# Kernel tuning notes

Measured on AMD Instinct MI355X. Metric: run time of the kernel, lower is better.

The kernel has to match this reference:

```python
import jax, jax.numpy as jnp
import numpy as np

D_MODEL = 1024
N_HEADS = 16


def setup_inputs() -> dict:
    key0 = jax.random.key(0)
    ks = jax.random.split(key0, 13)
    B, Lq, Lk, D = 2, 1024, 2048, D_MODEL
    scale = 0.02
    inp = {
        "query": jax.random.normal(ks[0], (B, Lq, D), jnp.float32),
        "key": jax.random.normal(ks[1], (B, Lk, D), jnp.float32),
        "value": jax.random.normal(ks[2], (B, Lk, D), jnp.float32),
        "mask": jax.random.randint(ks[3], (B, 1, Lq, Lk), 0, 2, jnp.int32),
        "attn_bias": jax.random.normal(ks[4], (B, N_HEADS, Lq, Lk), jnp.float32) * 0.1,
        "Wq": jax.random.normal(ks[5], (D, D), jnp.float32) * scale,
        "bq": jnp.zeros((D,), jnp.float32),
        "Wk": jax.random.normal(ks[6], (D, D), jnp.float32) * scale,
        "bk": jnp.zeros((D,), jnp.float32),
        "Wv": jax.random.normal(ks[7], (D, D), jnp.float32) * scale,
        "bv": jnp.zeros((D,), jnp.float32),
        "Wo": jax.random.normal(ks[8], (D, D), jnp.float32) * scale,
        "bo": jnp.zeros((D,), jnp.float32),
    }
    return inp


def reference(query, key, value, mask, attn_bias, Wq, bq, Wk, bk, Wv, bv, Wo, bo):
    B, Lq, D = query.shape
    Lk = key.shape[1]
    H = N_HEADS
    dh = D // H
    # projections (torch Linear: x @ W.T + b), then split heads -> [B,H,L,dh]
    Q = (query @ Wq.T + bq).reshape(B, Lq, H, dh).transpose(0, 2, 1, 3)
    K = (key @ Wk.T + bk).reshape(B, Lk, H, dh).transpose(0, 2, 1, 3)
    V = (value @ Wv.T + bv).reshape(B, Lk, H, dh).transpose(0, 2, 1, 3)
    scores = jnp.einsum("bhqd,bhkd->bhqk", Q, K) / jnp.sqrt(jnp.float32(dh))
    scores = scores + attn_bias
    scores = jnp.where(mask == 0, jnp.float32(-1e9), scores)
    attn = jax.nn.softmax(scores, axis=-1)  # dropout disabled (eval / p=0)
    out = jnp.einsum("bhqk,bhkd->bhqd", attn, V)
    out = out.transpose(0, 2, 1, 3).reshape(B, Lq, D)
    out = out @ Wo.T + bo
    return out, attn
```

## Files before the change

### kernel.cpp

```cpp
#include <hip/hip_runtime.h>
#include <hip/hip_bf16.h>

typedef __hip_bfloat16 bf16;
typedef __bf16  bf16x8 __attribute__((ext_vector_type(8)));
typedef float   f32x4  __attribute__((ext_vector_type(4)));

static constexpr int DMODEL = 1024;
static constexpr int NHEADS = 16;
static constexpr int DHEAD  = 64;
static constexpr int BATCH  = 2;
static constexpr int SLQ    = 1024;
static constexpr int SLK    = 2048;
static constexpr size_t OUTQ = (size_t)BATCH * SLQ * DMODEL;

__device__ __forceinline__ void stage8(unsigned short* dst, const bf16* src) {
    *(int4*)dst = *(const int4*)src;
}
__device__ __forceinline__ void stage8(unsigned short* dst, const float* src) {
    const float4 a = *(const float4*)(src);
    const float4 b = *(const float4*)(src + 4);
    bf16 h[8];
    h[0] = __float2bfloat16(a.x); h[1] = __float2bfloat16(a.y);
    h[2] = __float2bfloat16(a.z); h[3] = __float2bfloat16(a.w);
    h[4] = __float2bfloat16(b.x); h[5] = __float2bfloat16(b.y);
    h[6] = __float2bfloat16(b.z); h[7] = __float2bfloat16(b.w);
    *(int4*)dst = *(const int4*)h;
}

__device__ __forceinline__ void store_one(bf16* p, float v) { *p = __float2bfloat16(v); }
__device__ __forceinline__ void store_one(float* p, float v) { *p = v; }

template <typename TA, typename TB>
__device__ __forceinline__ void gemm_core(const TA* __restrict__ At, int lda,
                                          const TB* __restrict__ Bt, int ldb,
                                          int K, f32x4 acc[2][2])
{
    __shared__ __align__(16) unsigned short As[64][40];
    __shared__ __align__(16) unsigned short Bs[64][40];
    const int tid  = threadIdx.x;
    const int lane = tid & 63;
    const int wave = tid >> 6;
    const int wr   = (wave >> 1) * 32;
    const int wc   = (wave & 1) * 32;
    const int lrow = lane & 15;
    const int koff = (lane >> 4) * 8;
    const int srow   = tid >> 2;
    const int schunk = (tid & 3) * 8;

    for (int kt = 0; kt < K; kt += 32) {
        stage8(&As[srow][schunk], At + (size_t)srow * lda + kt + schunk);
        stage8(&Bs[srow][schunk], Bt + (size_t)srow * ldb + kt + schunk);
        __syncthreads();
        bf16x8 a0 = *(const bf16x8*)(&As[wr      + lrow][koff]);
        bf16x8 a1 = *(const bf16x8*)(&As[wr + 16 + lrow][koff]);
        bf16x8 b0 = *(const bf16x8*)(&Bs[wc      + lrow][koff]);
        bf16x8 b1 = *(const bf16x8*)(&Bs[wc + 16 + lrow][koff]);
        acc[0][0] = __builtin_amdgcn_mfma_f32_16x16x32_bf16(a0, b0, acc[0][0], 0, 0, 0);
        acc[0][1] = __builtin_amdgcn_mfma_f32_16x16x32_bf16(a0, b1, acc[0][1], 0, 0, 0);
        acc[1][0] = __builtin_amdgcn_mfma_f32_16x16x32_bf16(a1, b0, acc[1][0], 0, 0, 0);
        acc[1][1] = __builtin_amdgcn_mfma_f32_16x16x32_bf16(a1, b1, acc[1][1], 0, 0, 0);
        __syncthreads();
    }
}

template <typename TA, typename TC>
__global__ __launch_bounds__(256)
void k_proj(const TA* __restrict__ A, const float* __restrict__ W,
            const float* __restrict__ bias, TC* __restrict__ C, int K, int N)
{
    const int m0 = blockIdx.x * 64;
    const int n0 = blockIdx.y * 64;
    f32x4 z = {0.f, 0.f, 0.f, 0.f};
    f32x4 acc[2][2] = {{z, z}, {z, z}};
    gemm_core(A + (size_t)m0 * K, K, W + (size_t)n0 * K, K, K, acc);
    const int lane = threadIdx.x & 63;
    const int wave = threadIdx.x >> 6;
    const int wr = (wave >> 1) * 32, wc = (wave & 1) * 32;
#pragma unroll
    for (int i = 0; i < 2; ++i)
#pragma unroll
        for (int j = 0; j < 2; ++j) {
            const int col = n0 + wc + j * 16 + (lane & 15);
            const float bv = bias[col];
#pragma unroll
            for (int r = 0; r < 4; ++r) {
                const int row = m0 + wr + i * 16 + (lane >> 4) * 4 + r;
                store_one(&C[(size_t)row * N + col], acc[i][j][r] + bv);
            }
        }
}

__global__ __launch_bounds__(256)
void k_projV(const float* __restrict__ A, const float* __restrict__ W,
             const float* __restrict__ bias, bf16* __restrict__ Vt)
{
    const int m0 = blockIdx.x * 64;
    const int n0 = blockIdx.y * 64;
    f32x4 z = {0.f, 0.f, 0.f, 0.f};
    f32x4 acc[2][2] = {{z, z}, {z, z}};
    gemm_core(A + (size_t)m0 * DMODEL, DMODEL, W + (size_t)n0 * DMODEL, DMODEL, DMODEL, acc);
    const int lane = threadIdx.x & 63;
    const int wave = threadIdx.x >> 6;
    const int wr = (wave >> 1) * 32, wc = (wave & 1) * 32;
#pragma unroll
    for (int i = 0; i < 2; ++i)
#pragma unroll
        for (int j = 0; j < 2; ++j) {
            const int col = n0 + wc + j * 16 + (lane & 15);
            const float bv = bias[col];
            const int h = col >> 6, d = col & 63;
            const int mb = m0 + wr + i * 16 + (lane >> 4) * 4;
            const int b = mb >> 11;
            const int kk = mb & 2047;
            bf16* dst = Vt + ((size_t)(b * NHEADS + h) * DHEAD + d) * SLK + kk;
#pragma unroll
            for (int r = 0; r < 4; ++r)
                dst[r] = __float2bfloat16(acc[i][j][r] + bv);
        }
}

__global__ __launch_bounds__(256)
void k_attn(const bf16* __restrict__ Qp, const bf16* __restrict__ Kp,
            const float* __restrict__ bias, const int* __restrict__ mask,
            const bf16* __restrict__ Vt, float* __restrict__ attn,
            bf16* __restrict__ ctx)
{
    constexpr int SST = 2052;
    constexpr int PST = 520;

    __shared__ __align__(16) float S[16 * SST];
    __shared__ __align__(16) bf16  Pc[16 * PST];
    __shared__ float wmax[4][16], wsum[4][16];
    __shared__ float m_s[16], inv_s[16];

    const int qt = blockIdx.x, bh = blockIdx.y;
    const int b = bh >> 4, h = bh & 15;
    const int q0 = qt * 16;
    const int tid  = threadIdx.x;
    const int lane = tid & 63, w = tid >> 6;
    const int lr = lane & 15, lk = lane >> 4;

    const bf16* qb = Qp + ((size_t)(b * SLQ + q0 + lr)) * DMODEL + h * DHEAD + lk * 8;
    const bf16x8 a0 = *(const bf16x8*)qb;
    const bf16x8 a1 = *(const bf16x8*)(qb + 32);

    const bf16* kb = Kp + (size_t)b * SLK * DMODEL + h * DHEAD + lk * 8;
#pragma unroll 4
    for (int ct = 0; ct < 32; ++ct) {
        const int c0 = w * 512 + ct * 16;
        const bf16* kp = kb + (size_t)(c0 + lr) * DMODEL;
        bf16x8 b0 = *(const bf16x8*)kp;
        bf16x8 b1 = *(const bf16x8*)(kp + 32);
        f32x4 acc = {0.f, 0.f, 0.f, 0.f};
        acc = __builtin_amdgcn_mfma_f32_16x16x32_bf16(a0, b0, acc, 0, 0, 0);
        acc = __builtin_amdgcn_mfma_f32_16x16x32_bf16(a1, b1, acc, 0, 0, 0);
#pragma unroll
        for (int r = 0; r < 4; ++r)
            S[(lk * 4 + r) * SST + c0 + lr] = acc[r] * 0.125f;
    }

    for (int r = 0; r < 16; ++r) {
        float* sp = &S[r * SST + w * 512];
        const size_t brow = ((size_t)bh * SLQ + q0 + r) * SLK + w * 512 + lane * 4;
        const size_t mrow = ((size_t)b  * SLQ + q0 + r) * SLK + w * 512 + lane * 4;
        f32x4 v0 = *(const f32x4*)(sp + lane * 4);
        f32x4 v1 = *(const f32x4*)(sp + 256 + lane * 4);
        const float4 bb0 = *(const float4*)(bias + brow);
        const float4 bb1 = *(const float4*)(bias + brow + 256);
        const int4 mm0 = *(const int4*)(mask + mrow);
        const int4 mm1 = *(const int4*)(mask + mrow + 256);
        float s0 = (mm0.x == 0) ? -1e9f : v0[0] + bb0.x;
        float s1 = (mm0.y == 0) ? -1e9f : v0[1] + bb0.y;
        float s2 = (mm0.z == 0) ? -1e9f : v0[2] + bb0.z;
        float s3 = (mm0.w == 0) ? -1e9f : v0[3] + bb0.w;
        float s4 = (mm1.x == 0) ? -1e9f : v1[0] + bb1.x;
        float s5 = (mm1.y == 0) ? -1e9f : v1[1] + bb1.y;
        float s6 = (mm1.z == 0) ? -1e9f : v1[2] + bb1.z;
        float s7 = (mm1.w == 0) ? -1e9f : v1[3] + bb1.w;
        f32x4 w0 = {s0, s1, s2, s3};
        f32x4 w1 = {s4, s5, s6, s7};
        *(f32x4*)(sp + lane * 4)       = w0;
        *(f32x4*)(sp + 256 + lane * 4) = w1;

        float mx = fmaxf(fmaxf(fmaxf(s0, s1), fmaxf(s2, s3)),
                         fmaxf(fmaxf(s4, s5), fmaxf(s6, s7)));
        float l = __expf(s0 - mx) + __expf(s1 - mx) + __expf(s2 - mx) + __expf(s3 - mx)
                + __expf(s4 - mx) + __expf(s5 - mx) + __expf(s6 - mx) + __expf(s7 - mx);
        float mw = mx;
#pragma unroll
        for (int d = 1; d < 64; d <<= 1) mw = fmaxf(mw, __shfl_xor(mw, d));
        float lw = l * __expf(mx - mw);
#pragma unroll
        for (int d = 1; d < 64; d <<= 1) lw += __shfl_xor(lw, d);
        if (lane == 0) { wmax[w][r] = mw; wsum[w][r] = lw; }
    }
    __syncthreads();
    if (tid < 16) {
        const float m = fmaxf(fmaxf(wmax[0][tid], wmax[1][tid]),
                              fmaxf(wmax[2][tid], wmax[3][tid]));
        const float l = wsum[0][tid] * __expf(wmax[0][tid] - m)
                      + wsum[1][tid] * __expf(wmax[1][tid] - m)
                      + wsum[2][tid] * __expf(wmax[2][tid] - m)
                      + wsum[3][tid] * __expf(wmax[3][tid] - m);
        m_s[tid]   = m;
        inv_s[tid] = 1.0f / l;
    }
    __syncthreads();

    f32x4 pv = {0.f, 0.f, 0.f, 0.f};
    const bf16* vb = Vt + (size_t)bh * DHEAD * SLK + (size_t)(w * 16 + lr) * SLK + lk * 8;
    const int trow = tid >> 7;
    const int tcol = (tid & 127) * 4;
    for (int c = 0; c < 4; ++c) {
        const int ck0 = c * 512;
#pragma unroll
        for (int rp = 0; rp < 8; ++rp) {
            const int row = rp * 2 + trow;
            const f32x4 sv = *(const f32x4*)&S[row * SST + ck0 + tcol];
            const float m = m_s[row], inv = inv_s[row];
            const float p0 = __expf(sv[0] - m) * inv;
            const float p1 = __expf(sv[1] - m) * inv;
            const float p2 = __expf(sv[2] - m) * inv;
            const float p3 = __expf(sv[3] - m) * inv;
            const f32x4 pf = {p0, p1, p2, p3};
            __builtin_nontemporal_store(pf,
                (f32x4*)(attn + ((size_t)bh * SLQ + q0 + row) * SLK + ck0 + tcol));
            bf16 t4[4] = {__float2bfloat16(p0), __float2bfloat16(p1),
                          __float2bfloat16(p2), __float2bfloat16(p3)};
            *(int2*)&Pc[row * PST + tcol] = *(const int2*)t4;
        }
        __syncthreads();
        const bf16* vc = vb + ck0;
#pragma unroll
        for (int ks = 0; ks < 16; ++ks) {
            bf16x8 pa = *(const bf16x8*)&Pc[lr * PST + ks * 32 + lk * 8];
            bf16x8 vv = *(const bf16x8*)(vc + ks * 32);
            pv = __builtin_amdgcn_mfma_f32_16x16x32_bf16(pa, vv, pv, 0, 0, 0);
        }
        __syncthreads();
    }

    const int d = w * 16 + lr;
#pragma unroll
    for (int r = 0; r < 4; ++r) {
        const int q = lk * 4 + r;
        ctx[((size_t)(b * SLQ + q0 + q)) * DMODEL + h * DHEAD + d] =
            __float2bfloat16(pv[r]);
    }
}

extern "C" void kernel_launch(void* const* d_in, const int* in_sizes, int n_in,
                              void* d_out, int out_size, void* d_ws, size_t ws_size,
                              hipStream_t stream)
{
    const float* query = (const float*)d_in[0];
    const float* key   = (const float*)d_in[1];
    const float* value = (const float*)d_in[2];
    const int*   mask  = (const int*)d_in[3];
    const float* bias  = (const float*)d_in[4];
    const float* Wq = (const float*)d_in[5];
    const float* bq = (const float*)d_in[6];
    const float* Wk = (const float*)d_in[7];
    const float* bk = (const float*)d_in[8];
    const float* Wv = (const float*)d_in[9];
    const float* bv = (const float*)d_in[10];
    const float* Wo = (const float*)d_in[11];
    const float* bo = (const float*)d_in[12];

    float* out  = (float*)d_out;
    float* attn = out + OUTQ;

    bf16* Qp  = (bf16*)d_ws;
    bf16* ctx = (bf16*)d_ws;
    bf16* Kp  = (bf16*)d_out;
    bf16* Vt  = (bf16*)d_ws + (size_t)4 * 1024 * 1024;

    dim3 blk(256);

    k_proj<float, bf16><<<dim3(BATCH * SLQ / 64, DMODEL / 64), blk, 0, stream>>>(query, Wq, bq, Qp, DMODEL, DMODEL);
    k_proj<float, bf16><<<dim3(BATCH * SLK / 64, DMODEL / 64), blk, 0, stream>>>(key,   Wk, bk, Kp, DMODEL, DMODEL);
    k_projV<<<dim3(BATCH * SLK / 64, DMODEL / 64), blk, 0, stream>>>(value, Wv, bv, Vt);
    k_attn<<<dim3(SLQ / 16, BATCH * NHEADS), blk, 0, stream>>>(Qp, Kp, bias, mask, Vt, attn, ctx);
    k_proj<bf16, float><<<dim3(BATCH * SLQ / 64, DMODEL / 64), blk, 0, stream>>>(ctx, Wo, bo, out, DMODEL, DMODEL);
}
```

Before: 823.6 us.

## Run attention kernel with 1024 threads, one wave per query row

The attention block grows from 4 to 16 waves. Each wave computes a 128-column slice of QK^T, then owns one full query row for the bias, mask and softmax, which removes the cross-wave max/sum merge. The PV product is split across 4 K-groups per output d-slice, and the partial sums are reduced through shared memory. This raises parallelism per block to hide memory latency on the large bias, mask and attn traffic. In exchange it adds an extra reduction pass and barrier, and the __launch_bounds__(1024, 4) setting constrains registers.

```diff
diff --git a/kernel.cpp b/kernel.cpp
--- a/kernel.cpp
+++ b/kernel.cpp
@@ -119,7 +119,7 @@
         }
 }
 
-__global__ __launch_bounds__(256)
+__global__ __launch_bounds__(1024, 4)
 void k_attn(const bf16* __restrict__ Qp, const bf16* __restrict__ Kp,
             const float* __restrict__ bias, const int* __restrict__ mask,
             const bf16* __restrict__ Vt, float* __restrict__ attn,
@@ -130,7 +130,6 @@
 
     __shared__ __align__(16) float S[16 * SST];
     __shared__ __align__(16) bf16  Pc[16 * PST];
-    __shared__ float wmax[4][16], wsum[4][16];
     __shared__ float m_s[16], inv_s[16];
 
     const int qt = blockIdx.x, bh = blockIdx.y;
@@ -145,9 +144,9 @@
     const bf16x8 a1 = *(const bf16x8*)(qb + 32);
 
     const bf16* kb = Kp + (size_t)b * SLK * DMODEL + h * DHEAD + lk * 8;
-#pragma unroll 4
-    for (int ct = 0; ct < 32; ++ct) {
-        const int c0 = w * 512 + ct * 16;
+#pragma unroll 2
+    for (int ct = 0; ct < 8; ++ct) {
+        const int c0 = w * 128 + ct * 16;
         const bf16* kp = kb + (size_t)(c0 + lr) * DMODEL;
         bf16x8 b0 = *(const bf16x8*)kp;
         bf16x8 b1 = *(const bf16x8*)(kp + 32);
@@ -158,94 +157,93 @@
         for (int r = 0; r < 4; ++r)
             S[(lk * 4 + r) * SST + c0 + lr] = acc[r] * 0.125f;
     }
-
-    for (int r = 0; r < 16; ++r) {
-        float* sp = &S[r * SST + w * 512];
-        const size_t brow = ((size_t)bh * SLQ + q0 + r) * SLK + w * 512 + lane * 4;
-        const size_t mrow = ((size_t)b  * SLQ + q0 + r) * SLK + w * 512 + lane * 4;
-        f32x4 v0 = *(const f32x4*)(sp + lane * 4);
-        f32x4 v1 = *(const f32x4*)(sp + 256 + lane * 4);
-        const float4 bb0 = *(const float4*)(bias + brow);
-        const float4 bb1 = *(const float4*)(bias + brow + 256);
-        const int4 mm0 = *(const int4*)(mask + mrow);
-        const int4 mm1 = *(const int4*)(mask + mrow + 256);
-        float s0 = (mm0.x == 0) ? -1e9f : v0[0] + bb0.x;
-        float s1 = (mm0.y == 0) ? -1e9f : v0[1] + bb0.y;
-        float s2 = (mm0.z == 0) ? -1e9f : v0[2] + bb0.z;
-        float s3 = (mm0.w == 0) ? -1e9f : v0[3] + bb0.w;
-        float s4 = (mm1.x == 0) ? -1e9f : v1[0] + bb1.x;
-        float s5 = (mm1.y == 0) ? -1e9f : v1[1] + bb1.y;
-        float s6 = (mm1.z == 0) ? -1e9f : v1[2] + bb1.z;
-        float s7 = (mm1.w == 0) ? -1e9f : v1[3] + bb1.w;
-        f32x4 w0 = {s0, s1, s2, s3};
-        f32x4 w1 = {s4, s5, s6, s7};
-        *(f32x4*)(sp + lane * 4)       = w0;
-        *(f32x4*)(sp + 256 + lane * 4) = w1;
-
-        float mx = fmaxf(fmaxf(fmaxf(s0, s1), fmaxf(s2, s3)),
-                         fmaxf(fmaxf(s4, s5), fmaxf(s6, s7)));
-        float l = __expf(s0 - mx) + __expf(s1 - mx) + __expf(s2 - mx) + __expf(s3 - mx)
-                + __expf(s4 - mx) + __expf(s5 - mx) + __expf(s6 - mx) + __expf(s7 - mx);
-        float mw = mx;
-#pragma unroll
-        for (int d = 1; d < 64; d <<= 1) mw = fmaxf(mw, __shfl_xor(mw, d));
-        float lw = l * __expf(mx - mw);
-#pragma unroll
-        for (int d = 1; d < 64; d <<= 1) lw += __shfl_xor(lw, d);
-        if (lane == 0) { wmax[w][r] = mw; wsum[w][r] = lw; }
-    }
     __syncthreads();
-    if (tid < 16) {
-        const float m = fmaxf(fmaxf(wmax[0][tid], wmax[1][tid]),
-                              fmaxf(wmax[2][tid], wmax[3][tid]));
-        const float l = wsum[0][tid] * __expf(wmax[0][tid] - m)
-                      + wsum[1][tid] * __expf(wmax[1][tid] - m)
-                      + wsum[2][tid] * __expf(wmax[2][tid] - m)
-                      + wsum[3][tid] * __expf(wmax[3][tid] - m);
-        m_s[tid]   = m;
-        inv_s[tid] = 1.0f / l;
+
+    {
+        float* sp = &S[w * SST];
+        const size_t brow = ((size_t)bh * SLQ + q0 + w) * SLK;
+        const size_t mrow = ((size_t)b  * SLQ + q0 + w) * SLK;
+        float mx = -3.0e38f;
+#pragma unroll 2
+        for (int j = 0; j < 8; ++j) {
+            const int col = j * 256 + lane * 4;
+            f32x4 v = *(const f32x4*)(sp + col);
+            const float4 bb = *(const float4*)(bias + brow + col);
+            const int4  mm = *(const int4*)(mask + mrow + col);
+            float s0 = (mm.x == 0) ? -1e9f : v[0] + bb.x;
+            float s1 = (mm.y == 0) ? -1e9f : v[1] + bb.y;
+            float s2 = (mm.z == 0) ? -1e9f : v[2] + bb.z;
+            float s3 = (mm.w == 0) ? -1e9f : v[3] + bb.w;
+            f32x4 wv = {s0, s1, s2, s3};
+            *(f32x4*)(sp + col) = wv;
+            mx = fmaxf(mx, fmaxf(fmaxf(s0, s1), fmaxf(s2, s3)));
+        }
+#pragma unroll
+        for (int d = 1; d < 64; d <<= 1) mx = fmaxf(mx, __shfl_xor(mx, d));
+        float l = 0.f;
+#pragma unroll 2
+        for (int j = 0; j < 8; ++j) {
+            const int col = j * 256 + lane * 4;
+            const f32x4 v = *(const f32x4*)(sp + col);
+            l += __expf(v[0] - mx) + __expf(v[1] - mx)
+               + __expf(v[2] - mx) + __expf(v[3] - mx);
+        }
+#pragma unroll
+        for (int d = 1; d < 64; d <<= 1) l += __shfl_xor(l, d);
+        if (lane == 0) { m_s[w] = mx; inv_s[w] = 1.0f / l; }
     }
     __syncthreads();
 
     f32x4 pv = {0.f, 0.f, 0.f, 0.f};
-    const bf16* vb = Vt + (size_t)bh * DHEAD * SLK + (size_t)(w * 16 + lr) * SLK + lk * 8;
-    const int trow = tid >> 7;
-    const int tcol = (tid & 127) * 4;
+    const int g = w >> 2, dg = w & 3;
+    const bf16* vb = Vt + (size_t)bh * DHEAD * SLK + (size_t)(dg * 16 + lr) * SLK + lk * 8;
     for (int c = 0; c < 4; ++c) {
         const int ck0 = c * 512;
-#pragma unroll
-        for (int rp = 0; rp < 8; ++rp) {
-            const int row = rp * 2 + trow;
-            const f32x4 sv = *(const f32x4*)&S[row * SST + ck0 + tcol];
-            const float m = m_s[row], inv = inv_s[row];
-            const float p0 = __expf(sv[0] - m) * inv;
-            const float p1 = __expf(sv[1] - m) * inv;
-            const float p2 = __expf(sv[2] - m) * inv;
-            const float p3 = __expf(sv[3] - m) * inv;
-            const f32x4 pf = {p0, p1, p2, p3};
-            __builtin_nontemporal_store(pf,
-                (f32x4*)(attn + ((size_t)bh * SLQ + q0 + row) * SLK + ck0 + tcol));
-            bf16 t4[4] = {__float2bfloat16(p0), __float2bfloat16(p1),
-                          __float2bfloat16(p2), __float2bfloat16(p3)};
-            *(int2*)&Pc[row * PST + tcol] = *(const int2*)t4;
+        {
+            const int scol = lane * 8;
+            const float m = m_s[w], inv = inv_s[w];
+            const f32x4 s0 = *(const f32x4*)&S[w * SST + ck0 + scol];
+            const f32x4 s1 = *(const f32x4*)&S[w * SST + ck0 + scol + 4];
+            const f32x4 p0 = {__expf(s0[0] - m) * inv, __expf(s0[1] - m) * inv,
+                              __expf(s0[2] - m) * inv, __expf(s0[3] - m) * inv};
+            const f32x4 p1 = {__expf(s1[0] - m) * inv, __expf(s1[1] - m) * inv,
+                              __expf(s1[2] - m) * inv, __expf(s1[3] - m) * inv};
+            float* ap = attn + ((size_t)bh * SLQ + q0 + w) * SLK + ck0 + scol;
+            __builtin_nontemporal_store(p0, (f32x4*)ap);
+            __builtin_nontemporal_store(p1, (f32x4*)(ap + 4));
+            bf16 t8[8] = {__float2bfloat16(p0[0]), __float2bfloat16(p0[1]),
+                          __float2bfloat16(p0[2]), __float2bfloat16(p0[3]),
+                          __float2bfloat16(p1[0]), __float2bfloat16(p1[1]),
+                          __float2bfloat16(p1[2]), __float2bfloat16(p1[3])};
+            *(int4*)&Pc[w * PST + scol] = *(const int4*)t8;
         }
         __syncthreads();
         const bf16* vc = vb + ck0;
 #pragma unroll
-        for (int ks = 0; ks < 16; ++ks) {
-            bf16x8 pa = *(const bf16x8*)&Pc[lr * PST + ks * 32 + lk * 8];
-            bf16x8 vv = *(const bf16x8*)(vc + ks * 32);
+        for (int i = 0; i < 4; ++i) {
+            const int koff = (g * 4 + i) * 32;
+            bf16x8 pa = *(const bf16x8*)&Pc[lr * PST + koff + lk * 8];
+            bf16x8 vv = *(const bf16x8*)(vc + koff);
             pv = __builtin_amdgcn_mfma_f32_16x16x32_bf16(pa, vv, pv, 0, 0, 0);
         }
         __syncthreads();
     }
 
-    const int d = w * 16 + lr;
-#pragma unroll
-    for (int r = 0; r < 4; ++r) {
-        const int q = lk * 4 + r;
-        ctx[((size_t)(b * SLQ + q0 + q)) * DMODEL + h * DHEAD + d] =
-            __float2bfloat16(pv[r]);
+    float* rbuf = S;
+    *(f32x4*)&rbuf[(w * 64 + lane) * 4] = pv;
+    __syncthreads();
+    if (g == 0) {
+        f32x4 t = {0.f, 0.f, 0.f, 0.f};
+#pragma unroll
+        for (int gg = 0; gg < 4; ++gg)
+            t += *(const f32x4*)&rbuf[((gg * 4 + dg) * 64 + lane) * 4];
+        const int d = dg * 16 + lr;
+#pragma unroll
+        for (int r = 0; r < 4; ++r) {
+            const int q = lk * 4 + r;
+            ctx[((size_t)(b * SLQ + q0 + q)) * DMODEL + h * DHEAD + d] =
+                __float2bfloat16(t[r]);
+        }
     }
 }
 
@@ -280,6 +278,6 @@
     k_proj<float, bf16><<<dim3(BATCH * SLQ / 64, DMODEL / 64), blk, 0, stream>>>(query, Wq, bq, Qp, DMODEL, DMODEL);
     k_proj<float, bf16><<<dim3(BATCH * SLK / 64, DMODEL / 64), blk, 0, stream>>>(key,   Wk, bk, Kp, DMODEL, DMODEL);
     k_projV<<<dim3(BATCH * SLK / 64, DMODEL / 64), blk, 0, stream>>>(value, Wv, bv, Vt);
-    k_attn<<<dim3(SLQ / 16, BATCH * NHEADS), blk, 0, stream>>>(Qp, Kp, bias, mask, Vt, attn, ctx);
+    k_attn<<<dim3(SLQ / 16, BATCH * NHEADS), dim3(1024), 0, stream>>>(Qp, Kp, bias, mask, Vt, attn, ctx);
     k_proj<bf16, float><<<dim3(BATCH * SLQ / 64, DMODEL / 64), blk, 0, stream>>>(ctx, Wo, bo, out, DMODEL, DMODEL);
 }
```

After: 740.4 us. 1.11x faster.
